# Kernel optimization log

Measured on AMD Instinct MI355X. Metric: run time of the kernel, lower is better.

The kernel has to match this reference:

```python
import jax, jax.numpy as jnp
import numpy as np

B, T, R, NS = 16, 2048, 256, 4


def setup_inputs() -> dict:
    key = jax.random.key(0)
    ks = jax.random.split(key, 11)
    s = 1.0 / np.sqrt(R)
    inp = {
        "q": jax.random.normal(ks[0], (B, T, R), jnp.float32),
        "k": jax.random.normal(ks[1], (B, T, R), jnp.float32),
        "v": jax.random.normal(ks[2], (B, T, R), jnp.float32),
        "wq": jax.random.uniform(ks[3], (R, R), jnp.float32, -s, s),
        "bq": jax.random.uniform(ks[4], (R,), jnp.float32, -s, s),
        "wk": jax.random.uniform(ks[5], (R, R), jnp.float32, -s, s),
        "bk": jax.random.uniform(ks[6], (R,), jnp.float32, -s, s),
        "wv": jax.random.uniform(ks[7], (NS, R, R), jnp.float32, -s, s),
        "bv": jax.random.uniform(ks[8], (NS, R), jnp.float32, -s, s),
        "wp": jax.random.uniform(ks[9], (R,), jnp.float32, -s, s),
        "bp": jax.random.uniform(ks[10], (), jnp.float32, -s, s),
    }
    return inp


def reference(q, k, v, wq, bq, wk, bk, wv, bv, wp, bp):
    # linear projections (torch Linear: x @ W.T + b)
    qp = q @ wq.T + bq                                   # [B,T,R]
    kp = k @ wk.T + bk                                   # [B,T,R]
    # n_state value projections, stacked on dim 1 -> [B,NS,T,R]
    vs = jnp.einsum('btr,nor->bnto', v, wv) + bv[None, :, None, :]

    # scaled dot-product attention with tril + (score==0 -> -10000) mask quirk
    scale = 1.0 / jnp.sqrt(jnp.asarray(q.shape[-1], qp.dtype))
    score = jnp.einsum('btr,bsr->bts', qp, kp) * scale   # [B,T,T]
    score = jnp.tril(score)
    score = jnp.where(score == 0, jnp.asarray(-10000.0, score.dtype), score)
    attn = jax.nn.softmax(score, axis=-1)                # [B,T,T]

    # batched AV (original does a python loop over batch; same math)
    out = jnp.einsum('bts,bnsr->bntr', attn, vs)         # [B,NS,T,R]

    # similarity loss: 0.5 * sum |cov(proj_score[b])| averaged over batch
    proj = jnp.einsum('bntr,r->bnt', vs, wp) + bp        # [B,NS,T]

    def cov_abs_sum(X):  # X: [NS, T], rows = variables
        Xc = X - X.mean(axis=1, keepdims=True)
        c = (Xc @ Xc.T) / (X.shape[1] - 1)               # [NS,NS]
        return 0.5 * jnp.sum(jnp.abs(c))

    sim_loss = jnp.mean(jax.vmap(cov_abs_sum)(proj))
    return out, sim_loss
```

## Files before the change

### kernel.cpp

```cpp
#include <hip/hip_runtime.h>

#define B_  16
#define T_  2048
#define R_  256
#define NS_ 4

typedef unsigned short u16;
typedef __attribute__((ext_vector_type(8))) __bf16 bf16x8;
typedef __attribute__((ext_vector_type(4))) float f32x4;

__device__ __forceinline__ u16 f2bf(float f){
  union { float f; unsigned u; } x; x.f = f;
  unsigned r = x.u + 0x7FFFu + ((x.u >> 16) & 1u);
  return (u16)(r >> 16);
}
__device__ __forceinline__ float bf2f(u16 h){
  union { unsigned u; float f; } x; x.u = ((unsigned)h) << 16; return x.f;
}

__device__ __forceinline__ void async_cp16(const void* g, void* l){
  __builtin_amdgcn_global_load_lds((__attribute__((address_space(1))) void*)g,
                                   (__attribute__((address_space(3))) void*)l,
                                   16, 0, 0);
}

__global__ __launch_bounds__(256)
void cvt_kernel(const float* __restrict__ src, u16* __restrict__ dst, int n4){
  int i = blockIdx.x*256 + threadIdx.x;
  if (i >= n4) return;
  float4 f = ((const float4*)src)[i];
  ushort4 o;
  o.x = f2bf(f.x); o.y = f2bf(f.y); o.z = f2bf(f.z); o.w = f2bf(f.w);
  ((ushort4*)dst)[i] = o;
}

__global__ __launch_bounds__(256)
void zero_kernel(float* __restrict__ p, int n){
  int i = blockIdx.x*256 + threadIdx.x;
  if (i < n) p[i] = 0.0f;
}

__global__ __launch_bounds__(256)
void pzero_kernel(u16* __restrict__ P){
  int blk = blockIdx.x;
  int b = blk & 15, tT = blk >> 4;
  long long base = (long long)b*T_*T_ + (long long)(tT*256)*T_ + (tT*256 + 128);
  int r = threadIdx.x >> 1, h = threadIdx.x & 1;
  u16* p = P + base + (long long)r*T_ + h*64;
  uint4 z = {0u,0u,0u,0u};
  #pragma unroll
  for (int i=0;i<8;i++) ((uint4*)p)[i] = z;
}

__global__ __launch_bounds__(256, 2)
void gemm_nt_bias(const u16* __restrict__ A, const u16* __restrict__ Bm,
                  u16* __restrict__ C, const float* __restrict__ bias,
                  int lda, int ldb, int ldc, int K,
                  long long sAn, long long sBb, long long sCz,
                  int sBiasN, int biasMode)
{
  __shared__ __align__(16) u16 As[128*32];
  __shared__ __align__(16) u16 Bs[128*32];
  int tid = threadIdx.x;
  int lane = tid & 63, wave = tid >> 6;
  int z = blockIdx.z;
  int nIdx = z & 3, bIdx = z >> 2;
  A    += (long long)nIdx * sAn;
  Bm   += (long long)bIdx * sBb;
  C    += (long long)z * sCz;
  bias += (long long)nIdx * sBiasN;
  int mBase = blockIdx.y * 128;
  int nBase = blockIdx.x * 128;
  int wm = (wave >> 1) * 64, wn = (wave & 1) * 64;
  int quad = lane >> 4, lc = lane & 15;

  f32x4 acc[4][4];
  #pragma unroll
  for (int i=0;i<4;i++)
    #pragma unroll
    for (int j=0;j<4;j++) acc[i][j] = (f32x4){0.f,0.f,0.f,0.f};

  for (int k0=0; k0<K; k0+=32){
    #pragma unroll
    for (int r=0;r<2;r++){
      int c = r*256 + tid;
      int row = c >> 2, col = (c & 3)*8;
      async_cp16(A  + (long long)(mBase+row)*lda + k0 + col, (void*)(As + (r*256 + wave*64)*8));
      async_cp16(Bm + (long long)(nBase+row)*ldb + k0 + col, (void*)(Bs + (r*256 + wave*64)*8));
    }
    __syncthreads();
    bf16x8 af[4], bfr[4];
    #pragma unroll
    for (int i=0;i<4;i++){
      af[i]  = *(const bf16x8*)(As + (wm + i*16 + lc)*32 + quad*8);
      bfr[i] = *(const bf16x8*)(Bs + (wn + i*16 + lc)*32 + quad*8);
    }
    #pragma unroll
    for (int i=0;i<4;i++)
      #pragma unroll
      for (int j=0;j<4;j++)
        acc[i][j] = __builtin_amdgcn_mfma_f32_16x16x32_bf16(af[i], bfr[j], acc[i][j], 0,0,0);
    __syncthreads();
  }
  #pragma unroll
  for (int i=0;i<4;i++){
    #pragma unroll
    for (int j=0;j<4;j++){
      int colG = nBase + wn + j*16 + lc;
      float bc = (biasMode==0) ? bias[colG] : 0.0f;
      #pragma unroll
      for (int e=0;e<4;e++){
        int rowG = mBase + wm + i*16 + quad*4 + e;
        float val = acc[i][j][e] + ((biasMode==0) ? bc : bias[rowG]);
        C[(long long)rowG*ldc + colG] = f2bf(val);
      }
    }
  }
}

__global__ __launch_bounds__(256, 4)
void attn_kernel(const u16* __restrict__ qp, const u16* __restrict__ kp,
                 u16* __restrict__ P, float* __restrict__ lsum)
{
  __shared__ __align__(16) u16 Qs[64*32];
  __shared__ __align__(16) u16 Ks[128*32];
  int tid = threadIdx.x, lane = tid & 63, wave = tid >> 6;
  int b = blockIdx.y;
  int f = blockIdx.x;
  int t64 = 31;
  while (f >= (t64 >> 1) + 1){ f -= (t64 >> 1) + 1; t64--; }
  int sT = f;
  int tBase = t64 * 64;
  const u16* Q  = qp + ((long long)b*T_ + tBase) * R_;
  const u16* Kt = kp + (long long)b*T_*R_ + (long long)sT*128*R_;
  u16* Pb = P + (long long)b*T_*T_;
  const float scale = 0.0625f;
  int quad = lane >> 4, lc = lane & 15;
  int rowLoc = wave*16 + quad*4;

  f32x4 acc[8];
  #pragma unroll
  for (int j=0;j<8;j++) acc[j] = (f32x4){0.f,0.f,0.f,0.f};

  for (int k0=0;k0<R_;k0+=32){
    {
      int row = tid >> 2, col = (tid & 3)*8;
      async_cp16(Q + (long long)row*R_ + k0 + col, (void*)(Qs + (wave*64)*8));
    }
    #pragma unroll
    for (int r=0;r<2;r++){
      int c = r*256 + tid;
      int row = c >> 2, col = (c & 3)*8;
      async_cp16(Kt + (long long)row*R_ + k0 + col, (void*)(Ks + (r*256 + wave*64)*8));
    }
    __syncthreads();
    bf16x8 aq = *(const bf16x8*)(Qs + (wave*16 + lc)*32 + quad*8);
    #pragma unroll
    for (int j=0;j<8;j++){
      bf16x8 bk = *(const bf16x8*)(Ks + (j*16 + lc)*32 + quad*8);
      acc[j] = __builtin_amdgcn_mfma_f32_16x16x32_bf16(aq, bk, acc[j], 0,0,0);
    }
    __syncthreads();
  }

  int sCol0 = sT*128 + lc;
  #pragma unroll
  for (int e=0;e<4;e++){
    int t = tBase + rowLoc + e;
    long long ro = (long long)t * T_;
    float rs = 0.0f;
    #pragma unroll
    for (int j=0;j<8;j++){
      float v = acc[j][e]*scale;
      int s = sCol0 + j*16;
      if (s > t || v == 0.0f) v = -10000.0f;
      float p = __expf(v);
      rs += p;
      Pb[ro + s] = f2bf(p);
    }
    #pragma unroll
    for (int off=1; off<16; off<<=1)
      rs += __shfl_xor(rs, off, 64);
    if (lc == 0)
      atomicAdd(&lsum[b*T_ + t], rs);
  }
}

#define MF(A,Bx,C) __builtin_amdgcn_mfma_f32_16x16x32_bf16(A,Bx,C,0,0,0)
#define VM8 asm volatile("s_waitcnt vmcnt(8)" ::: "memory")
#define VM6 asm volatile("s_waitcnt vmcnt(6)" ::: "memory")
#define VM4 asm volatile("s_waitcnt vmcnt(4)" ::: "memory")
#define VM0 asm volatile("s_waitcnt vmcnt(0)" ::: "memory")
#define LGSB(N) do{ asm volatile("s_waitcnt lgkmcnt(" #N ")" ::: "memory"); \
                    __builtin_amdgcn_sched_barrier(0); }while(0)

#define STAGE_A(KT,KH) do { \
  const u16* sp_ = aG + (int)((KT)*64 + (KH)*32); \
  u16* dp_ = (u16*)lds + (((KT)&1)*16384 + (KH)*8192 + wave*512); \
  async_cp16(sp_ + stOff, dp_); \
  async_cp16(sp_ + stOff + 128*2048, dp_ + 4096); \
} while(0)
#define STAGE_B(KT,KH) do { \
  const u16* sp_ = bG + (int)((KT)*64 + (KH)*32); \
  u16* dp_ = (u16*)lds + (32768 + ((KT)&1)*16384 + (KH)*8192 + wave*512); \
  async_cp16(sp_ + stOff, dp_); \
  async_cp16(sp_ + stOff + 128*2048, dp_ + 4096); \
} while(0)

#define LDA_F(BUF,KH,CU,TI) (*(const bf16x8*)(&lds[(BUF)*16384 + (KH)*8192 + (rbA + (CU)*64 + (TI)*16)*32 + qSw]))
#define LDB_F(BUF,KH,JJ)    (*(const bf16x8*)(&lds[32768 + (BUF)*16384 + (KH)*8192 + (rbB + (JJ)*16)*32 + qSw]))

#define RD_A(D0,D1,D2,D3,BUF,KH,CU) do { \
  D0 = LDA_F(BUF,KH,CU,0); D1 = LDA_F(BUF,KH,CU,1); \
  D2 = LDA_F(BUF,KH,CU,2); D3 = LDA_F(BUF,KH,CU,3); } while(0)
#define RD_B(D0,D1,D2,D3,BUF,KH) do { \
  D0 = LDB_F(BUF,KH,0); D1 = LDB_F(BUF,KH,1); \
  D2 = LDB_F(BUF,KH,2); D3 = LDB_F(BUF,KH,3); } while(0)

#define MFG(CU,G,Ag,Q0,Q1,Q2,Q3) do { \
  acc[(CU)*4+(G)][0]=MF(Ag,Q0,acc[(CU)*4+(G)][0]); \
  acc[(CU)*4+(G)][1]=MF(Ag,Q1,acc[(CU)*4+(G)][1]); \
  acc[(CU)*4+(G)][2]=MF(Ag,Q2,acc[(CU)*4+(G)][2]); \
  acc[(CU)*4+(G)][3]=MF(Ag,Q3,acc[(CU)*4+(G)][3]); } while(0)

#define PH(CU,A0,A1,A2,A3,Q0,Q1,Q2,Q3,W3,W2,W1,W0,...) do { \
  __VA_ARGS__ \
  LGSB(W3); \
  __builtin_amdgcn_s_setprio(1); \
  MFG(CU,0,A0,Q0,Q1,Q2,Q3); \
  LGSB(W2); \
  MFG(CU,1,A1,Q0,Q1,Q2,Q3); \
  LGSB(W1); \
  MFG(CU,2,A2,Q0,Q1,Q2,Q3); \
  LGSB(W0); \
  MFG(CU,3,A3,Q0,Q1,Q2,Q3); \
  __builtin_amdgcn_s_setprio(0); \
  asm volatile("" ::: "memory"); \
  __builtin_amdgcn_s_barrier(); \
} while(0)

__global__ __launch_bounds__(512, 2)
void pv_kernel(const u16* __restrict__ P, const u16* __restrict__ VT,
               const float* __restrict__ lsum, float* __restrict__ out)
{
  __shared__ __align__(16) u16 lds[65536];
  int tid = threadIdx.x, lane = tid & 63, wave = tid >> 6;
  int f = blockIdx.x;
  int xcd = f & 7, s = f >> 3;
  int g = xcd + 8*(s >> 2);
  int jIdx = s & 3;
  int b = g & 15;
  int tT = 7 - (g >> 4);
  int t0abs = tT * 256;
  int nIt = 2*(tT + 1);

  const u16* aG = P  + (long long)b*T_*T_ + (long long)t0abs*T_;
  const u16* bG = VT + (long long)b*1024*T_ + (long long)(jIdx*256)*T_;

  int stRow = tid >> 2;
  int vSt = (stRow & 3) ^ ((stRow >> 2) & 3);
  int stOff = stRow*2048 + (((tid & 3) ^ vSt) << 3);

  int quad = lane >> 4, lc = lane & 15;
  int wm = wave >> 2, wn = wave & 3;
  int vlc = (lc & 3) ^ ((lc >> 2) & 3);
  int qSw = ((quad ^ vlc) << 3);
  int rbA = wm*128 + lc;
  int rbB = wn*64 + lc;

  f32x4 acc[8][4];
  #pragma unroll
  for (int i=0;i<8;i++)
    #pragma unroll
    for (int j=0;j<4;j++) acc[i][j] = (f32x4){0.f,0.f,0.f,0.f};
  bf16x8 fA0,fA1,fA2,fA3, gA0,gA1,gA2,gA3;
  bf16x8 bX0,bX1,bX2,bX3, bY0,bY1,bY2,bY3;

  STAGE_A(0,0); STAGE_B(0,0);
  STAGE_A(0,1); STAGE_B(0,1);
  STAGE_A(1,0); STAGE_B(1,0);
  VM8;
  __builtin_amdgcn_s_barrier();
  RD_B(bX0,bX1,bX2,bX3, 0,0);
  RD_A(fA0,fA1,fA2,fA3, 0,0,0);

  for (int j = 0; j < nIt-1; ++j){
    int k1 = 2*j+1, k2 = 2*j+2, k3 = 2*j+3;
    PH(0, fA0,fA1,fA2,fA3, bX0,bX1,bX2,bX3, 7,6,5,4,
       RD_A(gA0,gA1,gA2,gA3, 0,0,1); STAGE_A(k1,1); VM6; );
    PH(1, gA0,gA1,gA2,gA3, bX0,bX1,bX2,bX3, 11,10,9,8,
       RD_B(bY0,bY1,bY2,bY3, 0,1); RD_A(fA0,fA1,fA2,fA3, 0,1,0);
       STAGE_B(k1,1); );
    PH(0, fA0,fA1,fA2,fA3, bY0,bY1,bY2,bY3, 7,6,5,4,
       RD_A(gA0,gA1,gA2,gA3, 0,1,1); STAGE_A(k2,0); VM6; );
    PH(1, gA0,gA1,gA2,gA3, bY0,bY1,bY2,bY3, 11,10,9,8,
       RD_B(bX0,bX1,bX2,bX3, 1,0); RD_A(fA0,fA1,fA2,fA3, 1,0,0);
       STAGE_B(k2,0); );
    PH(0, fA0,fA1,fA2,fA3, bX0,bX1,bX2,bX3, 7,6,5,4,
       RD_A(gA0,gA1,gA2,gA3, 1,0,1); STAGE_A(k2,1); VM6; );
    PH(1, gA0,gA1,gA2,gA3, bX0,bX1,bX2,bX3, 11,10,9,8,
       RD_B(bY0,bY1,bY2,bY3, 1,1); RD_A(fA0,fA1,fA2,fA3, 1,1,0);
       STAGE_B(k2,1); );
    PH(0, fA0,fA1,fA2,fA3, bY0,bY1,bY2,bY3, 7,6,5,4,
       RD_A(gA0,gA1,gA2,gA3, 1,1,1); STAGE_A(k3,0); VM6; );
    PH(1, gA0,gA1,gA2,gA3, bY0,bY1,bY2,bY3, 11,10,9,8,
       RD_B(bX0,bX1,bX2,bX3, 0,0); RD_A(fA0,fA1,fA2,fA3, 0,0,0);
       STAGE_B(k3,0); );
  }
  {
    int kL = 2*nIt - 1;
    PH(0, fA0,fA1,fA2,fA3, bX0,bX1,bX2,bX3, 7,6,5,4,
       RD_A(gA0,gA1,gA2,gA3, 0,0,1); STAGE_A(kL,1); VM6; );
    PH(1, gA0,gA1,gA2,gA3, bX0,bX1,bX2,bX3, 11,10,9,8,
       RD_B(bY0,bY1,bY2,bY3, 0,1); RD_A(fA0,fA1,fA2,fA3, 0,1,0);
       STAGE_B(kL,1); );
    PH(0, fA0,fA1,fA2,fA3, bY0,bY1,bY2,bY3, 7,6,5,4,
       RD_A(gA0,gA1,gA2,gA3, 0,1,1); VM4; );
    PH(1, gA0,gA1,gA2,gA3, bY0,bY1,bY2,bY3, 11,10,9,8,
       RD_B(bX0,bX1,bX2,bX3, 1,0); RD_A(fA0,fA1,fA2,fA3, 1,0,0); );
    PH(0, fA0,fA1,fA2,fA3, bX0,bX1,bX2,bX3, 7,6,5,4,
       RD_A(gA0,gA1,gA2,gA3, 1,0,1); VM0; );
    PH(1, gA0,gA1,gA2,gA3, bX0,bX1,bX2,bX3, 11,10,9,8,
       RD_B(bY0,bY1,bY2,bY3, 1,1); RD_A(fA0,fA1,fA2,fA3, 1,1,0); );
    PH(0, fA0,fA1,fA2,fA3, bY0,bY1,bY2,bY3, 7,6,5,4,
       RD_A(gA0,gA1,gA2,gA3, 1,1,1); );
    PH(1, gA0,gA1,gA2,gA3, bY0,bY1,bY2,bY3, 3,2,1,0, );
  }

  const float* lrow = lsum + b*T_;
  #pragma unroll
  for (int i=0;i<8;i++){
    float rl[4];
    #pragma unroll
    for (int e=0;e<4;e++)
      rl[e] = __builtin_amdgcn_rcpf(lrow[t0abs + wm*128 + i*16 + quad*4 + e]);
    #pragma unroll
    for (int j2=0;j2<4;j2++){
      int rcol = wn*64 + j2*16 + lc;
      #pragma unroll
      for (int e=0;e<4;e++){
        int t = t0abs + wm*128 + i*16 + quad*4 + e;
        out[(((long long)b*NS_ + jIdx)*T_ + t)*R_ + rcol] = acc[i][j2][e] * rl[e];
      }
    }
  }
}

__global__ __launch_bounds__(256)
void proj_kernel(const u16* __restrict__ VT, const float* __restrict__ wp,
                 const float* __restrict__ bp, float* __restrict__ proj){
  int gid = blockIdx.x*256 + threadIdx.x;
  int bn = gid >> 11, t = gid & 2047;
  const u16* base = VT + (long long)bn*R_*T_ + t;
  float acc = bp[0];
  #pragma unroll 8
  for (int o=0;o<R_;o++)
    acc = fmaf(bf2f(base[(long long)o*T_]), wp[o], acc);
  proj[gid] = acc;
}

__global__ __launch_bounds__(256)
void loss_batch_kernel(const float* __restrict__ proj, float* __restrict__ partial){
  __shared__ float red[4][14];
  int tid = threadIdx.x, lane = tid & 63, wave = tid >> 6;
  int b = blockIdx.x;
  const float* pb = proj + b*NS_*T_;
  float s[14];
  #pragma unroll
  for (int kk=0;kk<14;kk++) s[kk]=0.0f;
  for (int t=tid; t<T_; t+=256){
    float x0 = pb[0*T_+t], x1 = pb[1*T_+t], x2 = pb[2*T_+t], x3 = pb[3*T_+t];
    s[0]+=x0; s[1]+=x1; s[2]+=x2; s[3]+=x3;
    s[4]+=x0*x0; s[5]+=x1*x0; s[6]+=x1*x1; s[7]+=x2*x0; s[8]+=x2*x1;
    s[9]+=x2*x2; s[10]+=x3*x0; s[11]+=x3*x1; s[12]+=x3*x2; s[13]+=x3*x3;
  }
  #pragma unroll
  for (int kk=0;kk<14;kk++){
    #pragma unroll
    for (int off=1; off<64; off<<=1)
      s[kk] += __shfl_xor(s[kk], off, 64);
  }
  if (lane == 0){
    #pragma unroll
    for (int kk=0;kk<14;kk++) red[wave][kk] = s[kk];
  }
  __syncthreads();
  if (tid == 0){
    float tot[14];
    #pragma unroll
    for (int kk=0;kk<14;kk++)
      tot[kk] = red[0][kk] + red[1][kk] + red[2][kk] + red[3][kk];
    const float invT  = 1.0f/(float)T_;
    const float invT1 = 1.0f/(float)(T_-1);
    float csum = 0.0f;
    #pragma unroll
    for (int n=0;n<4;n++){
      #pragma unroll
      for (int m=0;m<=n;m++){
        int id = n*(n+1)/2 + m;
        float c = (tot[4+id] - tot[n]*tot[m]*invT) * invT1;
        csum += (n==m) ? fabsf(c) : 2.0f*fabsf(c);
      }
    }
    partial[b] = 0.5f*csum;
  }
}

__global__ void loss_final_kernel(const float* __restrict__ partial,
                                  float* __restrict__ simOut){
  if (threadIdx.x == 0){
    float sim = 0.0f;
    #pragma unroll
    for (int b=0;b<B_;b++) sim += partial[b];
    simOut[0] = sim * (1.0f/(float)B_);
  }
}

extern "C" void kernel_launch(void* const* d_in, const int* in_sizes, int n_in,
                              void* d_out, int out_size, void* d_ws, size_t ws_size,
                              hipStream_t stream)
{
  const float* q  = (const float*)d_in[0];
  const float* k  = (const float*)d_in[1];
  const float* v  = (const float*)d_in[2];
  const float* wq = (const float*)d_in[3];
  const float* bq = (const float*)d_in[4];
  const float* wk = (const float*)d_in[5];
  const float* bk = (const float*)d_in[6];
  const float* wv = (const float*)d_in[7];
  const float* bv = (const float*)d_in[8];
  const float* wp = (const float*)d_in[9];
  const float* bp = (const float*)d_in[10];
  float* out = (float*)d_out;

  char* ws = (char*)d_ws;
  u16* qbf   = (u16*)(ws + 0);
  u16* kbf   = (u16*)(ws + 16777216);
  u16* vbf   = (u16*)(ws + 33554432);
  u16* wqbf  = (u16*)(ws + 50331648);
  u16* wkbf  = (u16*)(ws + 50462720);
  u16* wvbf  = (u16*)(ws + 50593792);
  u16* qpbf  = (u16*)(ws + 51118080);
  u16* kpbf  = (u16*)(ws + 67895296);
  u16* vtbf  = (u16*)(ws + 84672512);
  u16* pbuf  = (u16*)(ws + 151781376);
  float* prj = (float*)(ws + 285999104);
  float* lpart = (float*)(ws + 0);
  float* lsum  = (float*)(ws + 16777216);

  cvt_kernel<<<8192,256,0,stream>>>(q,  qbf, 2097152);
  cvt_kernel<<<8192,256,0,stream>>>(k,  kbf, 2097152);
  cvt_kernel<<<8192,256,0,stream>>>(v,  vbf, 2097152);
  cvt_kernel<<<64,  256,0,stream>>>(wq, wqbf, 16384);
  cvt_kernel<<<64,  256,0,stream>>>(wk, wkbf, 16384);
  cvt_kernel<<<256, 256,0,stream>>>(wv, wvbf, 65536);

  dim3 gq(2,256,1);
  gemm_nt_bias<<<gq,256,0,stream>>>(qbf, wqbf, qpbf, bq, 256,256,256,256, 0,0,0, 0, 0);
  gemm_nt_bias<<<gq,256,0,stream>>>(kbf, wkbf, kpbf, bk, 256,256,256,256, 0,0,0, 0, 0);
  dim3 gv(16,2,64);
  gemm_nt_bias<<<gv,256,0,stream>>>(wvbf, vbf, vtbf, bv, 256,256,2048,256,
                                    65536LL, 524288LL, 524288LL, 256, 1);

  zero_kernel<<<128,256,0,stream>>>(lsum, 32768);
  pzero_kernel<<<128,256,0,stream>>>(pbuf);
  dim3 ga(272,16,1);
  attn_kernel<<<ga,256,0,stream>>>(qpbf, kpbf, pbuf, lsum);

  pv_kernel<<<512,512,0,stream>>>(pbuf, vtbf, lsum, out);

  proj_kernel<<<512,256,0,stream>>>(vtbf, wp, bp, prj);
  loss_batch_kernel<<<16,256,0,stream>>>(prj, lpart);
  loss_final_kernel<<<1,64,0,stream>>>(lpart, out + 33554432);
}
```

Measured before the change: 472.0 us.

## Restage PV GEMM loads as full 64-wide K tiles with new swizzle

```diff
diff --git a/kernel.cpp b/kernel.cpp
--- a/kernel.cpp
+++ b/kernel.cpp
@@ -188,27 +188,30 @@
 
 #define MF(A,Bx,C) __builtin_amdgcn_mfma_f32_16x16x32_bf16(A,Bx,C,0,0,0)
 #define VM8 asm volatile("s_waitcnt vmcnt(8)" ::: "memory")
-#define VM6 asm volatile("s_waitcnt vmcnt(6)" ::: "memory")
-#define VM4 asm volatile("s_waitcnt vmcnt(4)" ::: "memory")
 #define VM0 asm volatile("s_waitcnt vmcnt(0)" ::: "memory")
 #define LGSB(N) do{ asm volatile("s_waitcnt lgkmcnt(" #N ")" ::: "memory"); \
                     __builtin_amdgcn_sched_barrier(0); }while(0)
-
-#define STAGE_A(KT,KH) do { \
-  const u16* sp_ = aG + (int)((KT)*64 + (KH)*32); \
-  u16* dp_ = (u16*)lds + (((KT)&1)*16384 + (KH)*8192 + wave*512); \
-  async_cp16(sp_ + stOff, dp_); \
-  async_cp16(sp_ + stOff + 128*2048, dp_ + 4096); \
+#define NOP ((void)0)
+
+#define STAGE2_A(KT) do { \
+  const u16* sp_ = aG + (int)((KT)*64); \
+  u16* dp_ = (u16*)lds + (((KT)&1)*16384) + wave*512; \
+  async_cp16(sp_ + stOff2,            dp_); \
+  async_cp16(sp_ + stOff2 +  64*2048, dp_ + 4096); \
+  async_cp16(sp_ + stOff2 + 128*2048, dp_ + 8192); \
+  async_cp16(sp_ + stOff2 + 192*2048, dp_ + 12288); \
 } while(0)
-#define STAGE_B(KT,KH) do { \
-  const u16* sp_ = bG + (int)((KT)*64 + (KH)*32); \
-  u16* dp_ = (u16*)lds + (32768 + ((KT)&1)*16384 + (KH)*8192 + wave*512); \
-  async_cp16(sp_ + stOff, dp_); \
-  async_cp16(sp_ + stOff + 128*2048, dp_ + 4096); \
+#define STAGE2_B(KT) do { \
+  const u16* sp_ = bG + (int)((KT)*64); \
+  u16* dp_ = (u16*)lds + (32768 + ((KT)&1)*16384) + wave*512; \
+  async_cp16(sp_ + stOff2,            dp_); \
+  async_cp16(sp_ + stOff2 +  64*2048, dp_ + 4096); \
+  async_cp16(sp_ + stOff2 + 128*2048, dp_ + 8192); \
+  async_cp16(sp_ + stOff2 + 192*2048, dp_ + 12288); \
 } while(0)
 
-#define LDA_F(BUF,KH,CU,TI) (*(const bf16x8*)(&lds[(BUF)*16384 + (KH)*8192 + (rbA + (CU)*64 + (TI)*16)*32 + qSw]))
-#define LDB_F(BUF,KH,JJ)    (*(const bf16x8*)(&lds[32768 + (BUF)*16384 + (KH)*8192 + (rbB + (JJ)*16)*32 + qSw]))
+#define LDA_F(BUF,KH,CU,TI) (*(const bf16x8*)(&lds[(BUF)*16384 + (rbA + (CU)*64 + (TI)*16)*64 + (KH)*32 + qSw2]))
+#define LDB_F(BUF,KH,JJ)    (*(const bf16x8*)(&lds[32768 + (BUF)*16384 + (rbB + (JJ)*16)*64 + (KH)*32 + qSw2]))
 
 #define RD_A(D0,D1,D2,D3,BUF,KH,CU) do { \
   D0 = LDA_F(BUF,KH,CU,0); D1 = LDA_F(BUF,KH,CU,1); \
@@ -223,8 +226,8 @@
   acc[(CU)*4+(G)][2]=MF(Ag,Q2,acc[(CU)*4+(G)][2]); \
   acc[(CU)*4+(G)][3]=MF(Ag,Q3,acc[(CU)*4+(G)][3]); } while(0)
 
-#define PH(CU,A0,A1,A2,A3,Q0,Q1,Q2,Q3,W3,W2,W1,W0,...) do { \
-  __VA_ARGS__ \
+#define PH(CU,A0,A1,A2,A3,Q0,Q1,Q2,Q3,W3,W2,W1,W0,PRE,POST) do { \
+  PRE; \
   LGSB(W3); \
   __builtin_amdgcn_s_setprio(1); \
   MFG(CU,0,A0,Q0,Q1,Q2,Q3); \
@@ -235,6 +238,7 @@
   LGSB(W0); \
   MFG(CU,3,A3,Q0,Q1,Q2,Q3); \
   __builtin_amdgcn_s_setprio(0); \
+  POST; \
   asm volatile("" ::: "memory"); \
   __builtin_amdgcn_s_barrier(); \
 } while(0)
@@ -257,14 +261,11 @@
   const u16* aG = P  + (long long)b*T_*T_ + (long long)t0abs*T_;
   const u16* bG = VT + (long long)b*1024*T_ + (long long)(jIdx*256)*T_;
 
-  int stRow = tid >> 2;
-  int vSt = (stRow & 3) ^ ((stRow >> 2) & 3);
-  int stOff = stRow*2048 + (((tid & 3) ^ vSt) << 3);
+  int stOff2 = (wave*8 + (lane>>3))*2048 + (((lane&7) ^ (((lane>>5)&1)<<1))*8);
 
   int quad = lane >> 4, lc = lane & 15;
   int wm = wave >> 2, wn = wave & 3;
-  int vlc = (lc & 3) ^ ((lc >> 2) & 3);
-  int qSw = ((quad ^ vlc) << 3);
+  int qSw2 = (quad ^ ((lc >> 1) & 2)) * 8;
   int rbA = wm*128 + lc;
   int rbB = wn*64 + lc;
 
@@ -276,55 +277,67 @@
   bf16x8 fA0,fA1,fA2,fA3, gA0,gA1,gA2,gA3;
   bf16x8 bX0,bX1,bX2,bX3, bY0,bY1,bY2,bY3;
 
-  STAGE_A(0,0); STAGE_B(0,0);
-  STAGE_A(0,1); STAGE_B(0,1);
-  STAGE_A(1,0); STAGE_B(1,0);
+  STAGE2_A(0); STAGE2_B(0);
+  STAGE2_A(1); STAGE2_B(1);
   VM8;
   __builtin_amdgcn_s_barrier();
   RD_B(bX0,bX1,bX2,bX3, 0,0);
   RD_A(fA0,fA1,fA2,fA3, 0,0,0);
 
-  for (int j = 0; j < nIt-1; ++j){
-    int k1 = 2*j+1, k2 = 2*j+2, k3 = 2*j+3;
-    PH(0, fA0,fA1,fA2,fA3, bX0,bX1,bX2,bX3, 7,6,5,4,
-       RD_A(gA0,gA1,gA2,gA3, 0,0,1); STAGE_A(k1,1); VM6; );
-    PH(1, gA0,gA1,gA2,gA3, bX0,bX1,bX2,bX3, 11,10,9,8,
-       RD_B(bY0,bY1,bY2,bY3, 0,1); RD_A(fA0,fA1,fA2,fA3, 0,1,0);
-       STAGE_B(k1,1); );
-    PH(0, fA0,fA1,fA2,fA3, bY0,bY1,bY2,bY3, 7,6,5,4,
-       RD_A(gA0,gA1,gA2,gA3, 0,1,1); STAGE_A(k2,0); VM6; );
+  {
+    PH(0, fA0,fA1,fA2,fA3, bX0,bX1,bX2,bX3, 7,6,5,4,
+       RD_A(gA0,gA1,gA2,gA3, 0,0,1), NOP);
+    PH(1, gA0,gA1,gA2,gA3, bX0,bX1,bX2,bX3, 11,10,9,8,
+       RD_B(bY0,bY1,bY2,bY3, 0,1); RD_A(fA0,fA1,fA2,fA3, 0,1,0), NOP);
+    PH(0, fA0,fA1,fA2,fA3, bY0,bY1,bY2,bY3, 7,6,5,4,
+       RD_A(gA0,gA1,gA2,gA3, 0,1,1), VM0);
     PH(1, gA0,gA1,gA2,gA3, bY0,bY1,bY2,bY3, 11,10,9,8,
-       RD_B(bX0,bX1,bX2,bX3, 1,0); RD_A(fA0,fA1,fA2,fA3, 1,0,0);
-       STAGE_B(k2,0); );
-    PH(0, fA0,fA1,fA2,fA3, bX0,bX1,bX2,bX3, 7,6,5,4,
-       RD_A(gA0,gA1,gA2,gA3, 1,0,1); STAGE_A(k2,1); VM6; );
-    PH(1, gA0,gA1,gA2,gA3, bX0,bX1,bX2,bX3, 11,10,9,8,
-       RD_B(bY0,bY1,bY2,bY3, 1,1); RD_A(fA0,fA1,fA2,fA3, 1,1,0);
-       STAGE_B(k2,1); );
-    PH(0, fA0,fA1,fA2,fA3, bY0,bY1,bY2,bY3, 7,6,5,4,
-       RD_A(gA0,gA1,gA2,gA3, 1,1,1); STAGE_A(k3,0); VM6; );
+       RD_B(bX0,bX1,bX2,bX3, 1,0); RD_A(fA0,fA1,fA2,fA3, 1,0,0), NOP);
+    PH(0, fA0,fA1,fA2,fA3, bX0,bX1,bX2,bX3, 7,6,5,4,
+       RD_A(gA0,gA1,gA2,gA3, 1,0,1); STAGE2_A(2), NOP);
+    PH(1, gA0,gA1,gA2,gA3, bX0,bX1,bX2,bX3, 11,10,9,8,
+       RD_B(bY0,bY1,bY2,bY3, 1,1); RD_A(fA0,fA1,fA2,fA3, 1,1,0); STAGE2_B(2), NOP);
+    PH(0, fA0,fA1,fA2,fA3, bY0,bY1,bY2,bY3, 7,6,5,4,
+       RD_A(gA0,gA1,gA2,gA3, 1,1,1), VM0);
     PH(1, gA0,gA1,gA2,gA3, bY0,bY1,bY2,bY3, 11,10,9,8,
-       RD_B(bX0,bX1,bX2,bX3, 0,0); RD_A(fA0,fA1,fA2,fA3, 0,0,0);
-       STAGE_B(k3,0); );
+       RD_B(bX0,bX1,bX2,bX3, 0,0); RD_A(fA0,fA1,fA2,fA3, 0,0,0), NOP);
+  }
+  for (int j = 1; j < nIt-1; ++j){
+    int o = 2*j+1, n0 = 2*j+2;
+    PH(0, fA0,fA1,fA2,fA3, bX0,bX1,bX2,bX3, 7,6,5,4,
+       RD_A(gA0,gA1,gA2,gA3, 0,0,1); STAGE2_A(o), NOP);
+    PH(1, gA0,gA1,gA2,gA3, bX0,bX1,bX2,bX3, 11,10,9,8,
+       RD_B(bY0,bY1,bY2,bY3, 0,1); RD_A(fA0,fA1,fA2,fA3, 0,1,0); STAGE2_B(o), NOP);
+    PH(0, fA0,fA1,fA2,fA3, bY0,bY1,bY2,bY3, 7,6,5,4,
+       RD_A(gA0,gA1,gA2,gA3, 0,1,1), VM0);
+    PH(1, gA0,gA1,gA2,gA3, bY0,bY1,bY2,bY3, 11,10,9,8,
+       RD_B(bX0,bX1,bX2,bX3, 1,0); RD_A(fA0,fA1,fA2,fA3, 1,0,0), NOP);
+    PH(0, fA0,fA1,fA2,fA3, bX0,bX1,bX2,bX3, 7,6,5,4,
+       RD_A(gA0,gA1,gA2,gA3, 1,0,1); STAGE2_A(n0), NOP);
+    PH(1, gA0,gA1,gA2,gA3, bX0,bX1,bX2,bX3, 11,10,9,8,
+       RD_B(bY0,bY1,bY2,bY3, 1,1); RD_A(fA0,fA1,fA2,fA3, 1,1,0); STAGE2_B(n0), NOP);
+    PH(0, fA0,fA1,fA2,fA3, bY0,bY1,bY2,bY3, 7,6,5,4,
+       RD_A(gA0,gA1,gA2,gA3, 1,1,1), VM0);
+    PH(1, gA0,gA1,gA2,gA3, bY0,bY1,bY2,bY3, 11,10,9,8,
+       RD_B(bX0,bX1,bX2,bX3, 0,0); RD_A(fA0,fA1,fA2,fA3, 0,0,0), NOP);
   }
   {
     int kL = 2*nIt - 1;
     PH(0, fA0,fA1,fA2,fA3, bX0,bX1,bX2,bX3, 7,6,5,4,
-       RD_A(gA0,gA1,gA2,gA3, 0,0,1); STAGE_A(kL,1); VM6; );
-    PH(1, gA0,gA1,gA2,gA3, bX0,bX1,bX2,bX3, 11,10,9,8,
-       RD_B(bY0,bY1,bY2,bY3, 0,1); RD_A(fA0,fA1,fA2,fA3, 0,1,0);
-       STAGE_B(kL,1); );
-    PH(0, fA0,fA1,fA2,fA3, bY0,bY1,bY2,bY3, 7,6,5,4,
-       RD_A(gA0,gA1,gA2,gA3, 0,1,1); VM4; );
+       RD_A(gA0,gA1,gA2,gA3, 0,0,1); STAGE2_A(kL), NOP);
+    PH(1, gA0,gA1,gA2,gA3, bX0,bX1,bX2,bX3, 11,10,9,8,
+       RD_B(bY0,bY1,bY2,bY3, 0,1); RD_A(fA0,fA1,fA2,fA3, 0,1,0); STAGE2_B(kL), NOP);
+    PH(0, fA0,fA1,fA2,fA3, bY0,bY1,bY2,bY3, 7,6,5,4,
+       RD_A(gA0,gA1,gA2,gA3, 0,1,1), VM0);
     PH(1, gA0,gA1,gA2,gA3, bY0,bY1,bY2,bY3, 11,10,9,8,
-       RD_B(bX0,bX1,bX2,bX3, 1,0); RD_A(fA0,fA1,fA2,fA3, 1,0,0); );
-    PH(0, fA0,fA1,fA2,fA3, bX0,bX1,bX2,bX3, 7,6,5,4,
-       RD_A(gA0,gA1,gA2,gA3, 1,0,1); VM0; );
-    PH(1, gA0,gA1,gA2,gA3, bX0,bX1,bX2,bX3, 11,10,9,8,
-       RD_B(bY0,bY1,bY2,bY3, 1,1); RD_A(fA0,fA1,fA2,fA3, 1,1,0); );
-    PH(0, fA0,fA1,fA2,fA3, bY0,bY1,bY2,bY3, 7,6,5,4,
-       RD_A(gA0,gA1,gA2,gA3, 1,1,1); );
-    PH(1, gA0,gA1,gA2,gA3, bY0,bY1,bY2,bY3, 3,2,1,0, );
+       RD_B(bX0,bX1,bX2,bX3, 1,0); RD_A(fA0,fA1,fA2,fA3, 1,0,0), NOP);
+    PH(0, fA0,fA1,fA2,fA3, bX0,bX1,bX2,bX3, 7,6,5,4,
+       RD_A(gA0,gA1,gA2,gA3, 1,0,1), NOP);
+    PH(1, gA0,gA1,gA2,gA3, bX0,bX1,bX2,bX3, 11,10,9,8,
+       RD_B(bY0,bY1,bY2,bY3, 1,1); RD_A(fA0,fA1,fA2,fA3, 1,1,0), NOP);
+    PH(0, fA0,fA1,fA2,fA3, bY0,bY1,bY2,bY3, 7,6,5,4,
+       RD_A(gA0,gA1,gA2,gA3, 1,1,1), NOP);
+    PH(1, gA0,gA1,gA2,gA3, bY0,bY1,bY2,bY3, 3,2,1,0, NOP, NOP);
   }
 
   const float* lrow = lsum + b*T_;
```

New measurement: 476.7 us. No clear change (+1.0%).
